# Optimization experiments

Hardware: AMD Instinct MI355X
Metric: run time of the kernel (lower is better)

Reference implementation:

```python
import jax, jax.numpy as jnp
import numpy as np

N, E = 20000, 4096
IN_DIM, DET_DIM, HID, OUT = 512, 256, 256, 2
HALF = HID // 2
EPS = 1e-6


def setup_inputs() -> dict:
    key = jax.random.key(0)
    ks = jax.random.split(key, 20)
    g = lambda k, shape, fan_in: jax.random.normal(k, shape, jnp.float32) / np.sqrt(fan_in)
    return {
        "x": jax.random.normal(ks[0], (N, IN_DIM), jnp.float32),
        "z": jax.random.normal(ks[1], (N, DET_DIM), jnp.float32),
        "incidence": jax.random.uniform(ks[2], (N, E), jnp.float32),
        "edge_weights": jax.random.uniform(ks[3], (E,), jnp.float32),
        "psi_w": g(ks[4], (IN_DIM, HALF), IN_DIM), "psi_b": jnp.zeros((HALF,), jnp.float32),
        "phi_w": g(ks[5], (DET_DIM, HALF), DET_DIM), "phi_b": jnp.zeros((HALF,), jnp.float32),
        "g1_w": g(ks[6], (2 * HALF, HID), 2 * HALF), "g1_b": jnp.zeros((HID,), jnp.float32),
        "g2_w": g(ks[7], (HID, HALF), HID), "g2_b": jnp.zeros((HALF,), jnp.float32),
        "th1": g(ks[8], (HALF, HID), HALF), "b1": jnp.zeros((HID,), jnp.float32),
        "th2": g(ks[9], (HID, HID), HID), "b2": jnp.zeros((HID,), jnp.float32),
        "out_w": g(ks[10], (HID, OUT), HID), "out_b": jnp.zeros((OUT,), jnp.float32),
    }


def hconv(X, H, w, theta, bias):
    # HGNN-style message passing: Dv^{-1/2} H W De^{-1} H^T Dv^{-1/2} (X theta) + b
    Xt = X @ theta                              # [N,F]
    De = H.sum(axis=0)                          # [E] edge degree
    Dv = H @ w                                  # [N] weighted node degree
    inv_sqrt_dv = jax.lax.rsqrt(jnp.maximum(Dv, EPS))[:, None]
    He = H.T @ (Xt * inv_sqrt_dv)               # [E,F] gather to hyperedges
    He = He * (w / jnp.maximum(De, EPS))[:, None]
    return (H @ He) * inv_sqrt_dv + bias        # scatter back to nodes


def reference(x, z, incidence, edge_weights,
              psi_w, psi_b, phi_w, phi_b,
              g1_w, g1_b, g2_w, g2_b,
              th1, b1, th2, b2, out_w, out_b):
    proj_x = x @ psi_w + psi_b                  # [N,HALF]
    proj_z = z @ phi_w + phi_b                  # [N,HALF]
    cat = jnp.concatenate([proj_x, proj_z], axis=1)
    gate = jax.nn.sigmoid(jax.nn.relu(cat @ g1_w + g1_b) @ g2_w + g2_b)
    fused = gate * proj_z + (1.0 - gate) * proj_x
    h = jax.nn.relu(hconv(fused, incidence, edge_weights, th1, b1))
    h = jax.nn.relu(hconv(h, incidence, edge_weights, th2, b2))
    logits = h @ out_w + out_b                  # [N,OUT]
    return logits, gate
```

## Files before the change

### kernel.cpp

```cpp
#include <hip/hip_runtime.h>
#include <hip/hip_bf16.h>


typedef __bf16 bf16_t;
typedef __attribute__((ext_vector_type(8))) __bf16 bf16x8;
typedef __attribute__((ext_vector_type(4))) __bf16 bf16x4;
typedef __attribute__((ext_vector_type(4))) float f32x4;

#define NN 20000
#define NE 4096
#define NNP 20480
#define AT_S 16
#define NEB 16
#define NNB 160

__device__ __forceinline__ f32x4 mfma16(bf16x8 a, bf16x8 b, f32x4 c) {
  return __builtin_amdgcn_mfma_f32_16x16x32_bf16(a, b, c, 0, 0, 0);
}

__global__ __launch_bounds__(256) void stats_cvt_kern(const float* __restrict__ H,
                                                      const float* __restrict__ w,
                                                      float* __restrict__ Dvp,
                                                      float* __restrict__ Dep,
                                                      bf16_t* __restrict__ Hbp) {
  __shared__ float dvl[128];
  __shared__ float deP[4][256];
  int t = threadIdx.x, l = t & 63, wv = t >> 6;
  long e0 = (long)blockIdx.x * 256;
  long n0 = (long)blockIdx.y * 128;
  long pbase = ((e0 >> 6) + (l >> 4)) * (long)NNP;
  int inner = (l & 15) * 4;
  f32x4 w4 = *(const f32x4*)(w + e0 + l * 4);
  f32x4 de; de[0] = de[1] = de[2] = de[3] = 0.f;
  #pragma unroll 4
  for (int i = 0; i < 32; ++i) {
    long row = n0 + wv * 32 + i;
    float s;
    if (row < NN) {
      f32x4 u = *(const f32x4*)(H + row * NE + e0 + l * 4);
      bf16x4 pk;
      #pragma unroll
      for (int j = 0; j < 4; ++j) pk[j] = (__bf16)u[j];
      *(bf16x4*)(Hbp + (pbase + row) * 64 + inner) = pk;
      de += u;
      s = u[0] * w4[0] + u[1] * w4[1] + u[2] * w4[2] + u[3] * w4[3];
    } else {
      bf16x4 z;
      #pragma unroll
      for (int j = 0; j < 4; ++j) z[j] = (__bf16)0.f;
      *(bf16x4*)(Hbp + (pbase + row) * 64 + inner) = z;
      s = 0.f;
    }
    #pragma unroll
    for (int m = 1; m < 64; m <<= 1) s += __shfl_xor(s, m);
    if (l == 0) dvl[wv * 32 + i] = s;
  }
  *(f32x4*)(&deP[wv][l * 4]) = de;
  __syncthreads();
  if (t < 128) Dvp[(long)blockIdx.x * NNP + n0 + t] = dvl[t];
  {
    float s = deP[0][t] + deP[1][t] + deP[2][t] + deP[3][t];
    Dep[(long)blockIdx.y * NE + e0 + t] = s;
  }
}

__global__ __launch_bounds__(256) void finalize_kern(const float* __restrict__ Dvp,
                                                     const float* __restrict__ Dep,
                                                     const float* __restrict__ w,
                                                     float* __restrict__ isd,
                                                     float* __restrict__ es) {
  int t = blockIdx.x * 256 + threadIdx.x;
  if (t < NN) {
    float s = 0.f;
    #pragma unroll 8
    for (int b = 0; b < NEB; ++b) s += Dvp[(long)b * NNP + t];
    isd[t] = rsqrtf(fmaxf(s, 1e-6f));
  }
  if (t < NE) {
    float s = 0.f;
    #pragma unroll 8
    for (int b = 0; b < NNB; ++b) s += Dep[(long)b * NE + t];
    es[t] = w[t] / fmaxf(s, 1e-6f);
  }
}

__global__ void cvtw_kern(const float* __restrict__ psi, const float* __restrict__ phi,
                          const float* __restrict__ g1,  const float* __restrict__ g2,
                          const float* __restrict__ th1, const float* __restrict__ th2,
                          bf16_t* dpsi, bf16_t* dphi, bf16_t* dg1, bf16_t* dg2,
                          bf16_t* dth1, bf16_t* dth2) {
  int t = blockIdx.x * 256 + threadIdx.x;
  if (t < 65536) {
    int nc = t >> 9, k = t & 511; dpsi[t] = (__bf16)psi[k * 128 + nc];
  } else if (t < 98304) {
    int i = t - 65536; int nc = i >> 8, k = i & 255; dphi[i] = (__bf16)phi[k * 128 + nc];
  } else if (t < 163840) {
    int i = t - 98304; int nc = i >> 8, k = i & 255; dg1[i] = (__bf16)g1[k * 256 + nc];
  } else if (t < 196608) {
    int i = t - 163840; int nc = i >> 8, k = i & 255; dg2[i] = (__bf16)g2[k * 128 + nc];
  } else if (t < 229376) {
    int i = t - 196608; int nc = i >> 7, k = i & 127; dth1[i] = (__bf16)th1[k * 256 + nc];
  } else if (t < 294912) {
    int i = t - 229376; int nc = i >> 8, k = i & 255; dth2[i] = (__bf16)th2[k * 256 + nc];
  }
}

enum { EPI_CAT = 0, EPI_RELU = 1, EPI_GATE = 2, EPI_Y = 3 };

template<bool AF32, int EPI>
__global__ __launch_bounds__(256) void gemm_node_kern(
    const void* __restrict__ Av, int lda, const bf16_t* __restrict__ Bt, int K,
    const float* __restrict__ bias, float* __restrict__ gate_out,
    bf16_t* __restrict__ dst, int ldc, const bf16_t* __restrict__ cat,
    const float* __restrict__ isd) {
  int tid = threadIdx.x, l = tid & 63, wv = tid >> 6;
  int lr = l & 15, lq = l >> 4;
  int hm = wv >> 1;
  int mo = blockIdx.x * 32 + hm * 16;
  int no = blockIdx.y * 128 + (wv & 1) * 64;
  f32x4 acc[4] = {};
  for (int k0 = 0; k0 < K; k0 += 32) {
    int row = mo + lr;
    bf16x8 a;
    if (row < NN) {
      if constexpr (AF32) {
        const float* ap = (const float*)Av + (long)row * lda + k0 + lq * 8;
        f32x4 u0 = *(const f32x4*)ap, u1 = *(const f32x4*)(ap + 4);
        #pragma unroll
        for (int j = 0; j < 4; ++j) { a[j] = (__bf16)u0[j]; a[j + 4] = (__bf16)u1[j]; }
      } else {
        a = *(const bf16x8*)((const bf16_t*)Av + (long)row * lda + k0 + lq * 8);
      }
    } else {
      #pragma unroll
      for (int j = 0; j < 8; ++j) a[j] = (__bf16)0.f;
    }
    #pragma unroll
    for (int ni = 0; ni < 4; ++ni) {
      bf16x8 b = *(const bf16x8*)(Bt + (long)(no + ni * 16 + lr) * K + k0 + lq * 8);
      acc[ni] = mfma16(a, b, acc[ni]);
    }
  }
  #pragma unroll
  for (int ni = 0; ni < 4; ++ni) {
    int colf = no + ni * 16 + lr;
    int rb = mo + lq * 4;
    f32x4 v = acc[ni];
    if constexpr (EPI == EPI_CAT) {
      float bs = bias[colf];
      for (int r = 0; r < 4; ++r) { int n = rb + r;
        if (n < NN) dst[(long)n * ldc + colf] = (__bf16)(v[r] + bs); }
    } else if constexpr (EPI == EPI_RELU) {
      float bs = bias[colf];
      for (int r = 0; r < 4; ++r) { int n = rb + r;
        if (n < NN) { float xx = v[r] + bs; dst[(long)n * ldc + colf] = (__bf16)(xx > 0.f ? xx : 0.f); } }
    } else if constexpr (EPI == EPI_GATE) {
      float bs = bias[colf];
      for (int r = 0; r < 4; ++r) {
        int n = rb + r;
        if (n < NN) {
          float g = 1.f / (1.f + __expf(-(v[r] + bs)));
          gate_out[(long)n * 128 + colf] = g;
          float px = (float)cat[(long)n * 256 + colf];
          float pz = (float)cat[(long)n * 256 + 128 + colf];
          dst[(long)n * 128 + colf] = (__bf16)(g * pz + (1.f - g) * px);
        }
      }
    } else {
      int fblk = (no >> 4) + ni;
      int nblk = blockIdx.x;
      int lanep = (hm * 2 + (lq >> 1)) * 16 + lr;
      bf16x4 pk;
      for (int r = 0; r < 4; ++r) {
        int nr = rb + r;
        float sc = (nr < NN) ? isd[nr] : 0.f;
        pk[r] = (__bf16)(v[r] * sc);
      }
      *(bf16x4*)(dst + (((long)fblk * 640 + nblk) * 64 + lanep) * 8 + (lq & 1) * 4) = pk;
    }
  }
}

__global__ __launch_bounds__(512) void at_gemm_kern(const bf16_t* __restrict__ Hbp,
                                                    const bf16_t* __restrict__ Yf,
                                                    bf16_t* __restrict__ part) {
  __shared__ bf16_t T[128 * 72];
  int t = threadIdx.x, l = t & 63, wv = t >> 6;
  int lr = l & 15, lq = l >> 4;
  int eh = wv >> 2, fq = wv & 3;
  int e0 = blockIdx.x * 128;
  int s0 = blockIdx.y * 20, s1 = s0 + 20;
  int rp = t >> 4;
  int ck = t & 15;
  f32x4 acc[4][4] = {};
  const bf16_t* src = Hbp + (((long)(e0 >> 6) + (ck >> 3)) * NNP + (long)s0 * 64 + 2 * rp) * 64
                          + (ck & 7) * 8;
  bf16x8 ra = *(const bf16x8*)src;
  bf16x8 rb = *(const bf16x8*)(src + 64);
  for (int s = s0; s < s1; ++s) {
    __syncthreads();
    #pragma unroll
    for (int j = 0; j < 8; ++j) {
      int jj = (j + ck) & 7;
      int el = ck * 8 + jj;
      unsigned lo = (unsigned)__builtin_bit_cast(unsigned short, (__bf16)ra[jj]);
      unsigned hi = (unsigned)__builtin_bit_cast(unsigned short, (__bf16)rb[jj]);
      *(unsigned*)(T + el * 72 + rp * 2) = lo | (hi << 16);
    }
    __syncthreads();
    if (s + 1 < s1) {
      src += 64 * 64;
      ra = *(const bf16x8*)src;
      rb = *(const bf16x8*)(src + 64);
    }
    #pragma unroll
    for (int k32 = 0; k32 < 2; ++k32) {
      bf16x8 a[4], b[4];
      #pragma unroll
      for (int ni = 0; ni < 4; ++ni)
        a[ni] = *(const bf16x8*)(T + (eh * 64 + ni * 16 + lr) * 72 + k32 * 32 + lq * 8);
      const bf16_t* bp = Yf + ((long)(s * 2 + k32) * 64 + l) * 8;
      #pragma unroll
      for (int ni = 0; ni < 4; ++ni)
        b[ni] = *(const bf16x8*)(bp + (long)(fq * 4 + ni) * 640 * 512);
      #pragma unroll
      for (int ae = 0; ae < 4; ++ae)
        #pragma unroll
        for (int bf = 0; bf < 4; ++bf)
          acc[ae][bf] = mfma16(a[ae], b[bf], acc[ae][bf]);
    }
  }
  bf16_t* pp = part + (long)blockIdx.y * (256 * 4096);
  #pragma unroll
  for (int ae = 0; ae < 4; ++ae) {
    int eblk16 = (e0 >> 4) + eh * 4 + ae;
    #pragma unroll
    for (int bf = 0; bf < 4; ++bf) {
      int fblk = fq * 4 + bf;
      f32x4 v = acc[ae][bf];
      bf16x4 pk;
      for (int r = 0; r < 4; ++r) pk[r] = (__bf16)v[r];
      *(bf16x4*)(pp + (((long)eblk16 * 16 + fblk) * 64 + l) * 4) = pk;
    }
  }
}

__global__ __launch_bounds__(256) void reduce_he(const bf16_t* __restrict__ part,
                                                 const float* __restrict__ es,
                                                 bf16_t* __restrict__ Hef) {
  int u = blockIdx.x * 256 + threadIdx.x;
  int lane = u & 63, tile = u >> 6;
  int fblk = tile & 15, eblk16 = tile >> 4;
  int lr = lane & 15, lq = lane >> 4;
  int e_base = eblk16 * 16 + lq * 4;
  float a0 = 0.f, a1 = 0.f, a2 = 0.f, a3 = 0.f;
  #pragma unroll
  for (int s = 0; s < AT_S; ++s) {
    bf16x4 v = *(const bf16x4*)(part + (long)s * (256 * 4096) + (long)u * 4);
    a0 += (float)v[0]; a1 += (float)v[1]; a2 += (float)v[2]; a3 += (float)v[3];
  }
  f32x4 e4 = *(const f32x4*)(es + e_base);
  bf16x4 pk;
  pk[0] = (__bf16)(a0 * e4[0]); pk[1] = (__bf16)(a1 * e4[1]);
  pk[2] = (__bf16)(a2 * e4[2]); pk[3] = (__bf16)(a3 * e4[3]);
  int eblk32 = eblk16 >> 1;
  int lanep = ((eblk16 & 1) * 2 + (lq >> 1)) * 16 + lr;
  long slot = (((long)fblk * 128 + eblk32) * 64 + lanep) * 8 + (lq & 1) * 4;
  *(bf16x4*)(Hef + slot) = pk;
}

template<int FLOG>
__global__ __launch_bounds__(512) void out_gemm_kern(const bf16_t* __restrict__ Hef,
                                                     const bf16_t* __restrict__ Hbp,
                                                     const float* __restrict__ isd,
                                                     const float* __restrict__ bias,
                                                     bf16_t* __restrict__ h,
                                                     const float* __restrict__ ow,
                                                     const float* __restrict__ ob,
                                                     float* __restrict__ out) {
  __shared__ bf16_t lbuf[2][4096];
  __shared__ float lgp[8][64][2];
  int t = threadIdx.x, l = t & 63, wv = t >> 6;
  int lr = l & 15, lq = l >> 4;
  long r0 = (long)blockIdx.x * 64;
  f32x4 acc[4][2] = {};
  const bf16_t* asrc = Hbp + (r0 + (wv >> 1) * 16 + lr) * 64 + (wv & 1) * 32 + lq * 8;
  const bf16_t* bbase = Hef + (long)l * 8;
  bf16x8 rg = *(const bf16x8*)asrc;
  int c = 0;
  for (int s = 0; s < 64; ++s) {
    *(bf16x8*)(&lbuf[c][wv * 512 + l * 8]) = rg;
    __syncthreads();
    if (s + 1 < 64) rg = *(const bf16x8*)(asrc + (long)(s + 1) * NNP * 64);
    #pragma unroll
    for (int k32 = 0; k32 < 2; ++k32) {
      bf16x8 a[4], b[2];
      #pragma unroll
      for (int mi = 0; mi < 4; ++mi)
        a[mi] = *(const bf16x8*)(&lbuf[c][(mi * 2 + k32) * 512 + l * 8]);
      int eblk = s * 2 + k32;
      #pragma unroll
      for (int ni = 0; ni < 2; ++ni)
        b[ni] = *(const bf16x8*)(bbase + ((long)(wv * 2 + ni) * 128 + eblk) * 512);
      #pragma unroll
      for (int mi = 0; mi < 4; ++mi) {
        acc[mi][0] = mfma16(a[mi], b[0], acc[mi][0]);
        acc[mi][1] = mfma16(a[mi], b[1], acc[mi][1]);
      }
    }
    c ^= 1;
  }
  #pragma unroll
  for (int mi = 0; mi < 4; ++mi) {
    long nb = r0 + mi * 16 + lq * 4;
    #pragma unroll
    for (int r = 0; r < 4; ++r) {
      long n = nb + r;
      float sd = (n < NN) ? isd[n] : 0.f;
      float a0 = 0.f, a1 = 0.f;
      #pragma unroll
      for (int ni = 0; ni < 2; ++ni) {
        int f = wv * 32 + ni * 16 + lr;
        float vv = acc[mi][ni][r] * sd + bias[f];
        vv = vv > 0.f ? vv : 0.f;
        if constexpr (!FLOG) {
          if (n < NN) h[n * 256 + f] = (__bf16)vv;
        } else {
          a0 += vv * ow[f * 2];
          a1 += vv * ow[f * 2 + 1];
        }
      }
      if constexpr (FLOG) {
        #pragma unroll
        for (int m = 1; m < 16; m <<= 1) { a0 += __shfl_xor(a0, m); a1 += __shfl_xor(a1, m); }
        if (lr == 0) {
          int rowl = mi * 16 + lq * 4 + r;
          lgp[wv][rowl][0] = a0;
          lgp[wv][rowl][1] = a1;
        }
      }
    }
  }
  if constexpr (FLOG) {
    __syncthreads();
    if (t < 64) {
      float s0 = 0.f, s1 = 0.f;
      #pragma unroll
      for (int wvi = 0; wvi < 8; ++wvi) { s0 += lgp[wvi][t][0]; s1 += lgp[wvi][t][1]; }
      long n = r0 + t;
      if (n < NN) {
        out[n * 2]     = s0 + ob[0];
        out[n * 2 + 1] = s1 + ob[1];
      }
    }
  }
}

extern "C" void kernel_launch(void* const* d_in, const int* in_sizes, int n_in,
                              void* d_out, int out_size, void* d_ws, size_t ws_size,
                              hipStream_t stream) {
  const float* x    = (const float*)d_in[0];
  const float* z    = (const float*)d_in[1];
  const float* H    = (const float*)d_in[2];
  const float* w    = (const float*)d_in[3];
  const float* psi_w = (const float*)d_in[4];
  const float* psi_b = (const float*)d_in[5];
  const float* phi_w = (const float*)d_in[6];
  const float* phi_b = (const float*)d_in[7];
  const float* g1_w  = (const float*)d_in[8];
  const float* g1_b  = (const float*)d_in[9];
  const float* g2_w  = (const float*)d_in[10];
  const float* g2_b  = (const float*)d_in[11];
  const float* th1   = (const float*)d_in[12];
  const float* b1    = (const float*)d_in[13];
  const float* th2   = (const float*)d_in[14];
  const float* b2    = (const float*)d_in[15];
  const float* out_w = (const float*)d_in[16];
  const float* out_b = (const float*)d_in[17];

  float* logits_out = (float*)d_out;
  float* gate_out   = logits_out + (size_t)NN * 2;

  char* p = (char*)d_ws;
  auto alloc = [&](size_t bytes) { char* r = p; p += (bytes + 255) & ~(size_t)255; return r; };
  float* Dvp  = (float*)alloc((size_t)NEB * NNP * 4);
  float* Dep  = (float*)alloc((size_t)NNB * NE * 4);
  float* isd  = (float*)alloc((size_t)NN * 4);
  float* es   = (float*)alloc((size_t)NE * 4);
  bf16_t* cat   = (bf16_t*)alloc((size_t)NN * 256 * 2);
  bf16_t* hid1  = (bf16_t*)alloc((size_t)NN * 256 * 2);
  bf16_t* fusedb= (bf16_t*)alloc((size_t)NN * 128 * 2);
  bf16_t* Yf    = (bf16_t*)alloc((size_t)16 * 640 * 512 * 2);
  bf16_t* Hef   = (bf16_t*)alloc((size_t)16 * 128 * 512 * 2);
  bf16_t* h     = (bf16_t*)alloc((size_t)NN * 256 * 2);
  bf16_t* pbuf  = (bf16_t*)alloc((size_t)AT_S * 256 * 4096 * 2);
  bf16_t* Hbp   = (bf16_t*)alloc((size_t)NNP * NE * 2);
  bf16_t* psi_wt = (bf16_t*)alloc(65536 * 2);
  bf16_t* phi_wt = (bf16_t*)alloc(32768 * 2);
  bf16_t* g1_wt  = (bf16_t*)alloc(65536 * 2);
  bf16_t* g2_wt  = (bf16_t*)alloc(32768 * 2);
  bf16_t* th1_wt = (bf16_t*)alloc(32768 * 2);
  bf16_t* th2_wt = (bf16_t*)alloc(65536 * 2);

  cvtw_kern<<<1152, 256, 0, stream>>>(psi_w, phi_w, g1_w, g2_w, th1, th2,
                                      psi_wt, phi_wt, g1_wt, g2_wt, th1_wt, th2_wt);
  stats_cvt_kern<<<dim3(NEB, NNB), 256, 0, stream>>>(H, w, Dvp, Dep, Hbp);
  finalize_kern<<<79, 256, 0, stream>>>(Dvp, Dep, w, isd, es);

  gemm_node_kern<true,  EPI_CAT ><<<dim3(625, 1), 256, 0, stream>>>(x, 512, psi_wt, 512, psi_b, nullptr, cat,       256, nullptr, nullptr);
  gemm_node_kern<true,  EPI_CAT ><<<dim3(625, 1), 256, 0, stream>>>(z, 256, phi_wt, 256, phi_b, nullptr, cat + 128, 256, nullptr, nullptr);
  gemm_node_kern<false, EPI_RELU><<<dim3(625, 2), 256, 0, stream>>>(cat, 256, g1_wt, 256, g1_b, nullptr, hid1, 256, nullptr, nullptr);
  gemm_node_kern<false, EPI_GATE><<<dim3(625, 1), 256, 0, stream>>>(hid1, 256, g2_wt, 256, g2_b, gate_out, fusedb, 128, cat, nullptr);

  gemm_node_kern<false, EPI_Y><<<dim3(640, 2), 256, 0, stream>>>(fusedb, 128, th1_wt, 128, nullptr, nullptr, Yf, 0, nullptr, isd);
  at_gemm_kern<<<dim3(32, AT_S), 512, 0, stream>>>(Hbp, Yf, pbuf);
  reduce_he<<<1024, 256, 0, stream>>>(pbuf, es, Hef);
  out_gemm_kern<0><<<320, 512, 0, stream>>>(Hef, Hbp, isd, b1, h, nullptr, nullptr, nullptr);

  gemm_node_kern<false, EPI_Y><<<dim3(640, 2), 256, 0, stream>>>(h, 256, th2_wt, 256, nullptr, nullptr, Yf, 0, nullptr, isd);
  at_gemm_kern<<<dim3(32, AT_S), 512, 0, stream>>>(Hbp, Yf, pbuf);
  reduce_he<<<1024, 256, 0, stream>>>(pbuf, es, Hef);
  out_gemm_kern<1><<<320, 512, 0, stream>>>(Hef, Hbp, isd, b2, nullptr, out_w, out_b, logits_out);

  (void)in_sizes; (void)n_in; (void)out_size; (void)ws_size;
}
```

Before: 597.5 us.

## Fuse gate GEMM with theta1 projection and out-GEMM with theta2 projection

Merges the gate GEMM and fused-feature computation with the X·theta1 projection into one kernel, keeping the fused tile in shared memory. It also fuses the first conv's output (relu'd h) directly into the theta2 projection inside out_gemm, which drops the h and fused buffers and two separate launches. This saves global round trips and launch overhead. In exchange it adds a larger shared-memory footprint in out_gemm (about 33KB for hl), which could reduce occupancy, and the fused kernels do redundant weight loads per block.

```diff
diff --git a/kernel.cpp b/kernel.cpp
--- a/kernel.cpp
+++ b/kernel.cpp
@@ -105,14 +105,12 @@
   }
 }
 
-enum { EPI_CAT = 0, EPI_RELU = 1, EPI_GATE = 2, EPI_Y = 3 };
+enum { EPI_CAT = 0, EPI_RELU = 1 };
 
 template<bool AF32, int EPI>
 __global__ __launch_bounds__(256) void gemm_node_kern(
     const void* __restrict__ Av, int lda, const bf16_t* __restrict__ Bt, int K,
-    const float* __restrict__ bias, float* __restrict__ gate_out,
-    bf16_t* __restrict__ dst, int ldc, const bf16_t* __restrict__ cat,
-    const float* __restrict__ isd) {
+    const float* __restrict__ bias, bf16_t* __restrict__ dst, int ldc) {
   int tid = threadIdx.x, l = tid & 63, wv = tid >> 6;
   int lr = l & 15, lq = l >> 4;
   int hm = wv >> 1;
@@ -146,38 +144,83 @@
     int colf = no + ni * 16 + lr;
     int rb = mo + lq * 4;
     f32x4 v = acc[ni];
-    if constexpr (EPI == EPI_CAT) {
-      float bs = bias[colf];
-      for (int r = 0; r < 4; ++r) { int n = rb + r;
-        if (n < NN) dst[(long)n * ldc + colf] = (__bf16)(v[r] + bs); }
-    } else if constexpr (EPI == EPI_RELU) {
-      float bs = bias[colf];
-      for (int r = 0; r < 4; ++r) { int n = rb + r;
-        if (n < NN) { float xx = v[r] + bs; dst[(long)n * ldc + colf] = (__bf16)(xx > 0.f ? xx : 0.f); } }
-    } else if constexpr (EPI == EPI_GATE) {
-      float bs = bias[colf];
-      for (int r = 0; r < 4; ++r) {
-        int n = rb + r;
-        if (n < NN) {
-          float g = 1.f / (1.f + __expf(-(v[r] + bs)));
-          gate_out[(long)n * 128 + colf] = g;
-          float px = (float)cat[(long)n * 256 + colf];
-          float pz = (float)cat[(long)n * 256 + 128 + colf];
-          dst[(long)n * 128 + colf] = (__bf16)(g * pz + (1.f - g) * px);
-        }
-      }
-    } else {
-      int fblk = (no >> 4) + ni;
-      int nblk = blockIdx.x;
-      int lanep = (hm * 2 + (lq >> 1)) * 16 + lr;
-      bf16x4 pk;
-      for (int r = 0; r < 4; ++r) {
-        int nr = rb + r;
-        float sc = (nr < NN) ? isd[nr] : 0.f;
-        pk[r] = (__bf16)(v[r] * sc);
-      }
-      *(bf16x4*)(dst + (((long)fblk * 640 + nblk) * 64 + lanep) * 8 + (lq & 1) * 4) = pk;
-    }
+    float bs = bias[colf];
+    for (int r = 0; r < 4; ++r) {
+      int n = rb + r;
+      if (n < NN) {
+        float xx = v[r] + bs;
+        if constexpr (EPI == EPI_RELU) xx = xx > 0.f ? xx : 0.f;
+        dst[(long)n * ldc + colf] = (__bf16)xx;
+      }
+    }
+  }
+}
+
+__global__ __launch_bounds__(256) void gate_y_kern(
+    const bf16_t* __restrict__ hid1, const bf16_t* __restrict__ g2w,
+    const float* __restrict__ g2b, const bf16_t* __restrict__ cat,
+    const bf16_t* __restrict__ th1w, const float* __restrict__ isd,
+    float* __restrict__ gate_out, bf16_t* __restrict__ Yf) {
+  __shared__ bf16_t fl[32 * 132];
+  int t = threadIdx.x, l = t & 63, wv = t >> 6;
+  int lr = l & 15, lq = l >> 4;
+  if (blockIdx.x >= 625) {
+    bf16x8 z;
+    #pragma unroll
+    for (int j = 0; j < 8; ++j) z[j] = (__bf16)0.f;
+    #pragma unroll
+    for (int i = 0; i < 4; ++i)
+      *(bf16x8*)(Yf + (((long)(wv + i * 4) * 640 + blockIdx.x) * 64 + l) * 8) = z;
+    return;
+  }
+  long n0 = (long)blockIdx.x * 32;
+  int hm = wv >> 1, nq = wv & 1;
+  int mo = hm * 16, no = nq * 64;
+  f32x4 acc[4] = {};
+  for (int k0 = 0; k0 < 256; k0 += 32) {
+    bf16x8 a = *(const bf16x8*)(hid1 + (n0 + mo + lr) * 256 + k0 + lq * 8);
+    #pragma unroll
+    for (int ni = 0; ni < 4; ++ni) {
+      bf16x8 b = *(const bf16x8*)(g2w + (long)(no + ni * 16 + lr) * 256 + k0 + lq * 8);
+      acc[ni] = mfma16(a, b, acc[ni]);
+    }
+  }
+  #pragma unroll
+  for (int ni = 0; ni < 4; ++ni) {
+    int colf = no + ni * 16 + lr;
+    float bs = g2b[colf];
+    #pragma unroll
+    for (int r = 0; r < 4; ++r) {
+      long n = n0 + mo + lq * 4 + r;
+      float g = 1.f / (1.f + __expf(-(acc[ni][r] + bs)));
+      gate_out[n * 128 + colf] = g;
+      float px = (float)cat[n * 256 + colf];
+      float pz = (float)cat[n * 256 + 128 + colf];
+      fl[(mo + lq * 4 + r) * 132 + colf] = (__bf16)(g * pz + (1.f - g) * px);
+    }
+  }
+  __syncthreads();
+  int hm2 = wv >> 1, f128 = (wv & 1) * 128;
+  f32x4 acc2[8] = {};
+  for (int k0 = 0; k0 < 128; k0 += 32) {
+    bf16x8 a = *(const bf16x8*)(fl + (hm2 * 16 + lr) * 132 + k0 + lq * 8);
+    #pragma unroll
+    for (int ni = 0; ni < 8; ++ni) {
+      bf16x8 b = *(const bf16x8*)(th1w + (long)(f128 + ni * 16 + lr) * 128 + k0 + lq * 8);
+      acc2[ni] = mfma16(a, b, acc2[ni]);
+    }
+  }
+  int lanep = (hm2 * 2 + (lq >> 1)) * 16 + lr;
+  #pragma unroll
+  for (int ni = 0; ni < 8; ++ni) {
+    int fblk = (f128 >> 4) + ni;
+    bf16x4 pk;
+    #pragma unroll
+    for (int r = 0; r < 4; ++r) {
+      long n = n0 + hm2 * 16 + lq * 4 + r;
+      pk[r] = (__bf16)(acc2[ni][r] * isd[n]);
+    }
+    *(bf16x4*)(Yf + (((long)fblk * 640 + blockIdx.x) * 64 + lanep) * 8 + (lq & 1) * 4) = pk;
   }
 }
 
@@ -269,17 +312,19 @@
   *(bf16x4*)(Hef + slot) = pk;
 }
 
-template<int FLOG>
+template<int CONV>
 __global__ __launch_bounds__(512) void out_gemm_kern(const bf16_t* __restrict__ Hef,
                                                      const bf16_t* __restrict__ Hbp,
                                                      const float* __restrict__ isd,
                                                      const float* __restrict__ bias,
-                                                     bf16_t* __restrict__ h,
+                                                     const bf16_t* __restrict__ th2w,
+                                                     bf16_t* __restrict__ Yf,
                                                      const float* __restrict__ ow,
                                                      const float* __restrict__ ob,
                                                      float* __restrict__ out) {
   __shared__ bf16_t lbuf[2][4096];
   __shared__ float lgp[8][64][2];
+  __shared__ bf16_t hl[64 * 260];
   int t = threadIdx.x, l = t & 63, wv = t >> 6;
   int lr = l & 15, lq = l >> 4;
   long r0 = (long)blockIdx.x * 64;
@@ -323,14 +368,14 @@
         int f = wv * 32 + ni * 16 + lr;
         float vv = acc[mi][ni][r] * sd + bias[f];
         vv = vv > 0.f ? vv : 0.f;
-        if constexpr (!FLOG) {
-          if (n < NN) h[n * 256 + f] = (__bf16)vv;
+        if constexpr (CONV == 1) {
+          hl[(mi * 16 + lq * 4 + r) * 260 + f] = (__bf16)vv;
         } else {
           a0 += vv * ow[f * 2];
           a1 += vv * ow[f * 2 + 1];
         }
       }
-      if constexpr (FLOG) {
+      if constexpr (CONV == 2) {
         #pragma unroll
         for (int m = 1; m < 16; m <<= 1) { a0 += __shfl_xor(a0, m); a1 += __shfl_xor(a1, m); }
         if (lr == 0) {
@@ -341,7 +386,38 @@
       }
     }
   }
-  if constexpr (FLOG) {
+  if constexpr (CONV == 1) {
+    __syncthreads();
+    int nh = wv >> 2, fq = wv & 3;
+    f32x4 acc2[2][4] = {};
+    for (int k0 = 0; k0 < 256; k0 += 32) {
+      bf16x8 a0v = *(const bf16x8*)(hl + (nh * 32 + lr) * 260 + k0 + lq * 8);
+      bf16x8 a1v = *(const bf16x8*)(hl + (nh * 32 + 16 + lr) * 260 + k0 + lq * 8);
+      #pragma unroll
+      for (int ni = 0; ni < 4; ++ni) {
+        bf16x8 b = *(const bf16x8*)(th2w + (long)(fq * 64 + ni * 16 + lr) * 256 + k0 + lq * 8);
+        acc2[0][ni] = mfma16(a0v, b, acc2[0][ni]);
+        acc2[1][ni] = mfma16(a1v, b, acc2[1][ni]);
+      }
+    }
+    long nblk = blockIdx.x * 2 + nh;
+    #pragma unroll
+    for (int mi = 0; mi < 2; ++mi) {
+      int lanep = (mi * 2 + (lq >> 1)) * 16 + lr;
+      #pragma unroll
+      for (int ni = 0; ni < 4; ++ni) {
+        int fblk = fq * 4 + ni;
+        bf16x4 pk;
+        #pragma unroll
+        for (int r = 0; r < 4; ++r) {
+          long n = r0 + nh * 32 + mi * 16 + lq * 4 + r;
+          float sc = (n < NN) ? isd[n] : 0.f;
+          pk[r] = (__bf16)(acc2[mi][ni][r] * sc);
+        }
+        *(bf16x4*)(Yf + (((long)fblk * 640 + nblk) * 64 + lanep) * 8 + (lq & 1) * 4) = pk;
+      }
+    }
+  } else {
     __syncthreads();
     if (t < 64) {
       float s0 = 0.f, s1 = 0.f;
@@ -389,10 +465,8 @@
   float* es   = (float*)alloc((size_t)NE * 4);
   bf16_t* cat   = (bf16_t*)alloc((size_t)NN * 256 * 2);
   bf16_t* hid1  = (bf16_t*)alloc((size_t)NN * 256 * 2);
-  bf16_t* fusedb= (bf16_t*)alloc((size_t)NN * 128 * 2);
   bf16_t* Yf    = (bf16_t*)alloc((size_t)16 * 640 * 512 * 2);
   bf16_t* Hef   = (bf16_t*)alloc((size_t)16 * 128 * 512 * 2);
-  bf16_t* h     = (bf16_t*)alloc((size_t)NN * 256 * 2);
   bf16_t* pbuf  = (bf16_t*)alloc((size_t)AT_S * 256 * 4096 * 2);
   bf16_t* Hbp   = (bf16_t*)alloc((size_t)NNP * NE * 2);
   bf16_t* psi_wt = (bf16_t*)alloc(65536 * 2);
@@ -407,20 +481,20 @@
   stats_cvt_kern<<<dim3(NEB, NNB), 256, 0, stream>>>(H, w, Dvp, Dep, Hbp);
   finalize_kern<<<79, 256, 0, stream>>>(Dvp, Dep, w, isd, es);
 
-  gemm_node_kern<true,  EPI_CAT ><<<dim3(625, 1), 256, 0, stream>>>(x, 512, psi_wt, 512, psi_b, nullptr, cat,       256, nullptr, nullptr);
-  gemm_node_kern<true,  EPI_CAT ><<<dim3(625, 1), 256, 0, stream>>>(z, 256, phi_wt, 256, phi_b, nullptr, cat + 128, 256, nullptr, nullptr);
-  gemm_node_kern<false, EPI_RELU><<<dim3(625, 2), 256, 0, stream>>>(cat, 256, g1_wt, 256, g1_b, nullptr, hid1, 256, nullptr, nullptr);
-  gemm_node_kern<false, EPI_GATE><<<dim3(625, 1), 256, 0, stream>>>(hid1, 256, g2_wt, 256, g2_b, gate_out, fusedb, 128, cat, nullptr);
-
-  gemm_node_kern<false, EPI_Y><<<dim3(640, 2), 256, 0, stream>>>(fusedb, 128, th1_wt, 128, nullptr, nullptr, Yf, 0, nullptr, isd);
+  gemm_node_kern<true,  EPI_CAT ><<<dim3(625, 1), 256, 0, stream>>>(x, 512, psi_wt, 512, psi_b, cat,       256);
+  gemm_node_kern<true,  EPI_CAT ><<<dim3(625, 1), 256, 0, stream>>>(z, 256, phi_wt, 256, phi_b, cat + 128, 256);
+  gemm_node_kern<false, EPI_RELU><<<dim3(625, 2), 256, 0, stream>>>(cat, 256, g1_wt, 256, g1_b, hid1, 256);
+  gate_y_kern<<<640, 256, 0, stream>>>(hid1, g2_wt, g2_b, cat, th1_wt, isd, gate_out, Yf);
+
   at_gemm_kern<<<dim3(32, AT_S), 512, 0, stream>>>(Hbp, Yf, pbuf);
   reduce_he<<<1024, 256, 0, stream>>>(pbuf, es, Hef);
-  out_gemm_kern<0><<<320, 512, 0, stream>>>(Hef, Hbp, isd, b1, h, nullptr, nullptr, nullptr);
-
-  gemm_node_kern<false, EPI_Y><<<dim3(640, 2), 256, 0, stream>>>(h, 256, th2_wt, 256, nullptr, nullptr, Yf, 0, nullptr, isd);
+  out_gemm_kern<1><<<320, 512, 0, stream>>>(Hef, Hbp, isd, b1, th2_wt, Yf,
+                                            nullptr, nullptr, nullptr);
+
   at_gemm_kern<<<dim3(32, AT_S), 512, 0, stream>>>(Hbp, Yf, pbuf);
   reduce_he<<<1024, 256, 0, stream>>>(pbuf, es, Hef);
-  out_gemm_kern<1><<<320, 512, 0, stream>>>(Hef, Hbp, isd, b2, nullptr, out_w, out_b, logits_out);
+  out_gemm_kern<2><<<320, 512, 0, stream>>>(Hef, Hbp, isd, b2, nullptr, nullptr,
+                                            out_w, out_b, logits_out);
 
   (void)in_sizes; (void)n_in; (void)out_size; (void)ws_size;
 }
```

Result: faster. 580.0 us (-2.9%).
